# Performance work log

Measured on AMD Instinct MI355X. Metric: run time of the kernel, lower is better.

The kernel has to match this reference:

```python
import jax, jax.numpy as jnp
import numpy as np

N_NODES = 100000
N_EDGES = 1000000
F_IN = 256
HID = 256
HID2 = 128
N_CLS = 2


def setup_inputs() -> dict:
    key = jax.random.key(0)
    ks = jax.random.split(key, 8)
    x = jax.random.normal(ks[0], (N_NODES, F_IN), dtype=jnp.float32)
    edge_index = jax.random.randint(ks[1], (2, N_EDGES), 0, N_NODES, dtype=jnp.int64)
    s = lambda k, shp: jax.random.normal(k, shp, dtype=jnp.float32) / np.sqrt(shp[0])
    return {
        "x": x,
        "edge_index": edge_index,
        "W1l": s(ks[2], (F_IN, HID)),
        "W1r": s(ks[3], (F_IN, HID)),
        "b1": jnp.zeros((HID,), jnp.float32),
        "W2l": s(ks[4], (HID, HID2)),
        "W2r": s(ks[5], (HID, HID2)),
        "b2": jnp.zeros((HID2,), jnp.float32),
        "Wc": s(ks[6], (HID2, N_CLS)),
        "bc": jnp.zeros((N_CLS,), jnp.float32),
    }


def _sage_conv(x, src, dst, deg_inv, Wl, Wr, b):
    # mean-aggregate neighbor (source) features at each destination node
    msg = x[src]                                              # [E, F]
    agg = jax.ops.segment_sum(msg, dst, num_segments=N_NODES)  # [N, F]
    mean = agg * deg_inv[:, None]                             # zero for isolated nodes
    return mean @ Wl + b + x @ Wr


def reference(x, edge_index, W1l, W1r, b1, W2l, W2r, b2, Wc, bc):
    src, dst = edge_index[0], edge_index[1]
    cnt = jax.ops.segment_sum(jnp.ones((N_EDGES,), x.dtype), dst, num_segments=N_NODES)
    deg_inv = jnp.where(cnt > 0, 1.0 / jnp.maximum(cnt, 1.0), 0.0)
    h = jax.nn.relu(_sage_conv(x, src, dst, deg_inv, W1l, W1r, b1))   # dropout is identity in eval
    h = jax.nn.relu(_sage_conv(h, src, dst, deg_inv, W2l, W2r, b2))
    logits = h @ Wc + bc
    return jax.nn.log_softmax(logits, axis=1)
```

## Files before the change

kernel.cpp:

```cpp
#include <hip/hip_runtime.h>
#include <hip/hip_bf16.h>

#define NN 100000
#define NE 1000000
#define MPAD 100096
#define MT64  1564
#define MTP64 1568
#define NG1   (MTP64 * 8)
#define NFB   (NE / 64)
#define NDB   ((NE + 255) / 256)
#define NCB   (MPAD / 8)

typedef __attribute__((ext_vector_type(8))) short bf16x8;
typedef __attribute__((ext_vector_type(4))) float f32x4;
typedef __attribute__((ext_vector_type(2))) float f32x2;
typedef __attribute__((ext_vector_type(8))) unsigned short us8;

static __device__ __forceinline__ float bf2f(unsigned short u){
  unsigned int x = ((unsigned int)u) << 16;
  return __uint_as_float(x);
}
static __device__ __forceinline__ unsigned short f2bf(float f){
  unsigned int x = __float_as_uint(f);
  unsigned int r = (x + 0x7fffu + ((x >> 16) & 1u)) >> 16;
  return (unsigned short)r;
}
static __device__ __forceinline__ void addv(float* acc, us8 v){
  #pragma unroll
  for (int k = 0; k < 8; k++) acc[k] += bf2f(v[k]);
}
static __device__ __forceinline__ unsigned char f2fp8(float f){
  unsigned int u = __float_as_uint(f);
  unsigned int s = (u >> 24) & 0x80u;
  float av = fabsf(f);
  if (av >= 448.f) return (unsigned char)(s | 0x7Eu);
  if (av < 0.015625f){
    int m = (int)(av * 512.0f + 0.5f);
    return (unsigned char)(s | (unsigned)m);
  }
  unsigned int au = u & 0x7FFFFFFFu;
  unsigned int r = au + 0x7FFFFu + ((au >> 20) & 1u);
  return (unsigned char)(s | ((r >> 20) - 960u));
}
#if !__has_builtin(__builtin_amdgcn_cvt_pk_f32_fp8)
static __device__ __forceinline__ float fp8tof(unsigned char b){
  unsigned int s = ((unsigned int)(b & 0x80u)) << 24;
  unsigned int e = (b >> 3) & 0xFu, m = b & 7u;
  float v = (e == 0) ? ((float)m * 0.001953125f)
                     : __uint_as_float(((e + 120u) << 23) | (m << 20));
  return __uint_as_float(__float_as_uint(v) | s);
}
#endif
static __device__ __forceinline__ void addq(float* acc, uint2 v){
#if __has_builtin(__builtin_amdgcn_cvt_pk_f32_fp8)
  f32x2 p0 = __builtin_amdgcn_cvt_pk_f32_fp8((int)v.x, false);
  f32x2 p1 = __builtin_amdgcn_cvt_pk_f32_fp8((int)v.x, true);
  f32x2 p2 = __builtin_amdgcn_cvt_pk_f32_fp8((int)v.y, false);
  f32x2 p3 = __builtin_amdgcn_cvt_pk_f32_fp8((int)v.y, true);
  acc[0] += p0[0]; acc[1] += p0[1]; acc[2] += p1[0]; acc[3] += p1[1];
  acc[4] += p2[0]; acc[5] += p2[1]; acc[6] += p3[0]; acc[7] += p3[1];
#else
  unsigned int a = v.x, b = v.y;
  acc[0] += fp8tof(a & 0xFF);         acc[1] += fp8tof((a >> 8) & 0xFF);
  acc[2] += fp8tof((a >> 16) & 0xFF); acc[3] += fp8tof(a >> 24);
  acc[4] += fp8tof(b & 0xFF);         acc[5] += fp8tof((b >> 8) & 0xFF);
  acc[6] += fp8tof((b >> 16) & 0xFF); acc[7] += fp8tof(b >> 24);
#endif
}
static __device__ __forceinline__ void gld16(const void* g, void* l){
  __builtin_amdgcn_global_load_lds((const __attribute__((address_space(1))) void*)g,
                                   (__attribute__((address_space(3))) void*)l, 16, 0, 0);
}


__global__ __launch_bounds__(256)
void k_dc(const int* __restrict__ dst, int* __restrict__ cnt,
          const float* __restrict__ x, unsigned short* __restrict__ xb,
          const float* __restrict__ W1l, const float* __restrict__ W1r,
          const float* __restrict__ W2l, const float* __restrict__ W2r,
          unsigned short* __restrict__ Bt1, unsigned short* __restrict__ Bt2)
{
  const int bid = blockIdx.x, t = threadIdx.x;
  int role, idx;
  if (bid < 2 * NDB){
    role = bid & 1;
    idx = bid >> 1;
  } else if (bid < NDB + NCB){
    role = 0; idx = bid - NDB;
  } else {
    role = 2; idx = bid - NDB - NCB;
  }

  if (role == 1){
    int e = idx * 256 + t;
    if (e < NE) atomicAdd(&cnt[dst[e]], 1);
  } else if (role == 0){
    size_t i = ((size_t)idx * 256 + t) * 8;
    if (i >= (size_t)MPAD * 256) return;
    int row = (int)(i >> 8);
    us8 o;
    if (row < NN){
      const float4* p = (const float4*)(x + i);
      float4 a = p[0], b = p[1];
      o[0]=f2bf(a.x); o[1]=f2bf(a.y); o[2]=f2bf(a.z); o[3]=f2bf(a.w);
      o[4]=f2bf(b.x); o[5]=f2bf(b.y); o[6]=f2bf(b.z); o[7]=f2bf(b.w);
    } else {
      #pragma unroll
      for (int j = 0; j < 8; j++) o[j] = 0;
    }
    *(us8*)(xb + i) = o;
  } else {
    int i = idx * 256 + t;
    if (i < 512 * 256){
      int n = i >> 8, k = i & 255;
      float v = (n < 256) ? W1l[k * 256 + n] : W1r[k * 256 + (n - 256)];
      Bt1[n * 256 + k] = f2bf(v);
    }
    if (i < 256 * 256){
      int n = i >> 8, k = i & 255;
      float v = (n < 128) ? W2l[k * 128 + n] : W2r[k * 128 + (n - 128)];
      Bt2[n * 256 + k] = f2bf(v);
    }
  }
}


__global__ void k_chunk_sum(const int* __restrict__ cnt, int* __restrict__ partials, int N){
  __shared__ int sw[16];
  int b = blockIdx.x, t = threadIdx.x;
  int i = b * 1024 + t;
  int v = (i < N) ? cnt[i] : 0;
  #pragma unroll
  for (int off = 32; off; off >>= 1) v += __shfl_xor(v, off);
  int lane = t & 63, w = t >> 6;
  if (lane == 0) sw[w] = v;
  __syncthreads();
  if (t < 16){
    int s = sw[t];
    #pragma unroll
    for (int off = 8; off; off >>= 1) s += __shfl_xor(s, off);
    if (t == 0) partials[b] = s;
  }
}

__global__ void k_chunk_scan(const int* __restrict__ cnt, const int* __restrict__ partials,
                             int nchunk,
                             int* __restrict__ offs, int* __restrict__ cursor,
                             float* __restrict__ deginv, int N){
  __shared__ int sd[1024];
  __shared__ int sp[128];
  int b = blockIdx.x, t = threadIdx.x;
  if (t < 128) sp[t] = (t < b && t < nchunk) ? partials[t] : 0;
  int i = b * 1024 + t;
  int v = (i < N) ? cnt[i] : 0;
  sd[t] = v;
  __syncthreads();
  #pragma unroll
  for (int off = 64; off; off >>= 1){
    if (t < off) sp[t] += sp[t + off];
    __syncthreads();
  }
  for (int off = 1; off < 1024; off <<= 1){
    int x = (t >= off) ? sd[t - off] : 0;
    __syncthreads();
    sd[t] += x;
    __syncthreads();
  }
  if (i < N){
    int excl = sp[0] + sd[t] - v;
    offs[i] = excl;
    cursor[i] = excl;
    deginv[i] = (v > 0) ? (1.0f / (float)v) : 0.0f;
  }
}


__global__ __launch_bounds__(64)
void k_fg(const unsigned short* __restrict__ A,
          const unsigned short* __restrict__ Bt,
          unsigned short* __restrict__ R1,
          unsigned char* __restrict__ Q8,
          const int* __restrict__ src, const int* __restrict__ dst,
          int* __restrict__ cursor, int* __restrict__ csr)
{
  __shared__ __align__(16) unsigned short lA[64 * 64];
  __shared__ __align__(16) unsigned short lB[64 * 64];
  const int bid = blockIdx.x;
  const int lane = threadIdx.x & 63;

  bool isg; int idx;
  if (bid < 2 * NG1){
    isg = (bid & 15) < 8;
    idx = ((bid >> 4) << 3) + (bid & 7);
  } else {
    isg = false; idx = bid - NG1;
  }

  if (!isg){
    int e = idx * 64 + lane;
    if (e < NE){
      int p = atomicAdd(&cursor[dst[e]], 1);
      csr[p] = src[e];
    }
    return;
  }

  const int xcd = idx & 7, j = idx >> 3;
  const int mt  = xcd * (MTP64 / 8) + (j >> 3);
  if (mt >= MT64) return;
  const int nt  = j & 7;
  const int m0  = mt * 64;
  const int n0  = nt * 64;

  f32x4 acc[4][4] = {};
  const int srow = lane >> 3;
  const int sc   = (lane & 7) ^ ((lane >> 3) & 7);

  for (int kt = 0; kt < 4; ++kt){
    asm volatile("s_waitcnt lgkmcnt(0)" ::: "memory");
    #pragma unroll
    for (int s = 0; s < 8; ++s){
      int row = s * 8 + srow;
      gld16(A  + (size_t)(m0 + row) * 256 + kt * 64 + sc * 8, &lA[s * 512]);
      gld16(Bt + (size_t)(n0 + row) * 256 + kt * 64 + sc * 8, &lB[s * 512]);
    }
    asm volatile("s_waitcnt vmcnt(0)" ::: "memory");
    __builtin_amdgcn_sched_barrier(0);
    #pragma unroll
    for (int ks = 0; ks < 2; ++ks){
      bf16x8 av[4], bv[4];
      const int kc = ks * 4 + (lane >> 4);
      #pragma unroll
      for (int m = 0; m < 4; m++){
        int r = m * 16 + (lane & 15);
        av[m] = *(const bf16x8*)&lA[r * 64 + ((kc ^ (r & 7)) << 3)];
      }
      #pragma unroll
      for (int n = 0; n < 4; n++){
        int c = n * 16 + (lane & 15);
        bv[n] = *(const bf16x8*)&lB[c * 64 + ((kc ^ (c & 7)) << 3)];
      }
      #pragma unroll
      for (int m = 0; m < 4; m++)
        #pragma unroll
        for (int n = 0; n < 4; n++)
          acc[m][n] = __builtin_amdgcn_mfma_f32_16x16x32_bf16(av[m], bv[n], acc[m][n], 0, 0, 0);
    }
  }

  const int crow0 = m0 + (lane >> 4) * 4;
  const int ccol0 = n0 + (lane & 15);
  if (n0 < 256){
    #pragma unroll
    for (int m = 0; m < 4; m++){
      #pragma unroll
      for (int r = 0; r < 4; r++){
        size_t rowoff = (size_t)(crow0 + m * 16 + r) * 256;
        #pragma unroll
        for (int n = 0; n < 4; n++)
          Q8[rowoff + ccol0 + n * 16] = f2fp8(acc[m][n][r]);
      }
    }
  } else {
    const int cbase = ccol0 - 256;
    #pragma unroll
    for (int m = 0; m < 4; m++){
      #pragma unroll
      for (int r = 0; r < 4; r++){
        size_t rowoff = (size_t)(crow0 + m * 16 + r) * 256;
        #pragma unroll
        for (int n = 0; n < 4; n++)
          R1[rowoff + cbase + n * 16] = f2bf(acc[m][n][r]);
      }
    }
  }
}


template<int NTL2>
__global__ __launch_bounds__(64)
void k_gemm(const unsigned short* __restrict__ A,
            const unsigned short* __restrict__ Bt,
            unsigned short* __restrict__ C)
{
  const int bid = blockIdx.x;
  const int xcd = bid & 7, j = bid >> 3;
  const int mt  = xcd * (MTP64 / 8) + (j >> NTL2);
  if (mt >= MT64) return;
  const int nt  = j & ((1 << NTL2) - 1);
  const int m0  = mt * 64;
  const int n0  = nt * 64;
  const int Nout = 64 << NTL2;

  __shared__ __align__(16) unsigned short lA[64 * 64];
  __shared__ __align__(16) unsigned short lB[64 * 64];
  const int lane = threadIdx.x & 63;

  f32x4 acc[4][4] = {};
  const int srow = lane >> 3;
  const int sc   = (lane & 7) ^ ((lane >> 3) & 7);

  for (int kt = 0; kt < 4; ++kt){
    asm volatile("s_waitcnt lgkmcnt(0)" ::: "memory");
    #pragma unroll
    for (int s = 0; s < 8; ++s){
      int row = s * 8 + srow;
      gld16(A  + (size_t)(m0 + row) * 256 + kt * 64 + sc * 8, &lA[s * 512]);
      gld16(Bt + (size_t)(n0 + row) * 256 + kt * 64 + sc * 8, &lB[s * 512]);
    }
    asm volatile("s_waitcnt vmcnt(0)" ::: "memory");
    __builtin_amdgcn_sched_barrier(0);
    #pragma unroll
    for (int ks = 0; ks < 2; ++ks){
      bf16x8 av[4], bv[4];
      const int kc = ks * 4 + (lane >> 4);
      #pragma unroll
      for (int m = 0; m < 4; m++){
        int r = m * 16 + (lane & 15);
        av[m] = *(const bf16x8*)&lA[r * 64 + ((kc ^ (r & 7)) << 3)];
      }
      #pragma unroll
      for (int n = 0; n < 4; n++){
        int c = n * 16 + (lane & 15);
        bv[n] = *(const bf16x8*)&lB[c * 64 + ((kc ^ (c & 7)) << 3)];
      }
      #pragma unroll
      for (int m = 0; m < 4; m++)
        #pragma unroll
        for (int n = 0; n < 4; n++)
          acc[m][n] = __builtin_amdgcn_mfma_f32_16x16x32_bf16(av[m], bv[n], acc[m][n], 0, 0, 0);
    }
  }

  const int crow0 = m0 + (lane >> 4) * 4;
  const int ccol0 = n0 + (lane & 15);
  #pragma unroll
  for (int m = 0; m < 4; m++){
    #pragma unroll
    for (int r = 0; r < 4; r++){
      size_t rowoff = (size_t)(crow0 + m * 16 + r) * Nout;
      #pragma unroll
      for (int n = 0; n < 4; n++)
        C[rowoff + ccol0 + n * 16] = f2bf(acc[m][n][r]);
    }
  }
}


__global__ void k_agg1(const unsigned char* __restrict__ Q8,
                       const unsigned short* __restrict__ R1,
                       const float* __restrict__ b1,
                       const int* __restrict__ offs, const int* __restrict__ cnt,
                       const float* __restrict__ deginv,
                       const int* __restrict__ csr,
                       unsigned short* __restrict__ h, int N)
{
  int wv = threadIdx.x >> 6, lane = threadIdx.x & 63;
  int n = blockIdx.x * 4 + wv;
  if (n >= N) return;
  int beg = offs[n], d = cnt[n];
  const int g = lane >> 5;
  const int cl = lane & 31;
  const unsigned char* Qb = Q8 + cl * 8;

  float acc[8];
  #pragma unroll
  for (int k = 0; k < 8; k++) acc[k] = 0.f;

  for (int w0 = 0; w0 < d; w0 += 64){
    int wlen = min(d - w0, 64);
    int idx = 0;
    if (lane < wlen) idx = csr[beg + w0 + lane];
    int nIter = (wlen + 15) >> 4;
    for (int t = 0; t < nIter; t++){
      int e0 = t * 16 + g;
      int s0 = __shfl(idx, e0);
      int s1 = __shfl(idx, e0 + 2);
      int s2 = __shfl(idx, e0 + 4);
      int s3 = __shfl(idx, e0 + 6);
      int s4 = __shfl(idx, e0 + 8);
      int s5 = __shfl(idx, e0 + 10);
      int s6 = __shfl(idx, e0 + 12);
      int s7 = __shfl(idx, e0 + 14);
      uint2 v0 = *(const uint2*)(Qb + (size_t)s0 * 256);
      uint2 v1 = *(const uint2*)(Qb + (size_t)s1 * 256);
      uint2 v2 = *(const uint2*)(Qb + (size_t)s2 * 256);
      uint2 v3 = *(const uint2*)(Qb + (size_t)s3 * 256);
      uint2 v4 = *(const uint2*)(Qb + (size_t)s4 * 256);
      uint2 v5 = *(const uint2*)(Qb + (size_t)s5 * 256);
      uint2 v6 = *(const uint2*)(Qb + (size_t)s6 * 256);
      uint2 v7 = *(const uint2*)(Qb + (size_t)s7 * 256);
      if (e0 < wlen)      addq(acc, v0);
      if (e0 + 2 < wlen)  addq(acc, v1);
      if (e0 + 4 < wlen)  addq(acc, v2);
      if (e0 + 6 < wlen)  addq(acc, v3);
      if (e0 + 8 < wlen)  addq(acc, v4);
      if (e0 + 10 < wlen) addq(acc, v5);
      if (e0 + 12 < wlen) addq(acc, v6);
      if (e0 + 14 < wlen) addq(acc, v7);
    }
  }
  #pragma unroll
  for (int k = 0; k < 8; k++) acc[k] += __shfl_xor(acc[k], 32);

  if (lane < 32){
    float di = deginv[n];
    us8 rv = *(const us8*)(R1 + (size_t)n * 256 + cl * 8);
    float4 b0 = *(const float4*)(b1 + cl * 8);
    float4 b4 = *(const float4*)(b1 + cl * 8 + 4);
    float bb[8] = {b0.x, b0.y, b0.z, b0.w, b4.x, b4.y, b4.z, b4.w};
    us8 o;
    #pragma unroll
    for (int k = 0; k < 8; k++)
      o[k] = f2bf(fmaxf(acc[k] * di + bf2f(rv[k]) + bb[k], 0.f));
    *(us8*)(h + (size_t)n * 256 + cl * 8) = o;
  }
}


__global__ void k_agg2cls(const unsigned short* __restrict__ C2,
                          const float* __restrict__ b2,
                          const float* __restrict__ Wc,
                          const float* __restrict__ bc,
                          const int* __restrict__ offs, const int* __restrict__ cnt,
                          const float* __restrict__ deginv,
                          const int* __restrict__ csr,
                          float* __restrict__ out, int N)
{
  int wv = threadIdx.x >> 6, lane = threadIdx.x & 63;
  int n = blockIdx.x * 4 + wv;
  if (n >= N) return;
  int beg = offs[n], d = cnt[n];
  const int g = lane >> 4;
  const int cl = lane & 15;

  float acc[8];
  #pragma unroll
  for (int k = 0; k < 8; k++) acc[k] = 0.f;

  for (int w0 = 0; w0 < d; w0 += 64){
    int wlen = min(d - w0, 64);
    int idx = 0;
    if (lane < wlen) idx = csr[beg + w0 + lane];
    int nIter = (wlen + 31) >> 5;
    for (int t = 0; t < nIter; t++){
      int e0 = t * 32 + g;
      int s0 = __shfl(idx, e0);
      int s1 = __shfl(idx, e0 + 4);
      int s2 = __shfl(idx, e0 + 8);
      int s3 = __shfl(idx, e0 + 12);
      int s4 = __shfl(idx, e0 + 16);
      int s5 = __shfl(idx, e0 + 20);
      int s6 = __shfl(idx, e0 + 24);
      int s7 = __shfl(idx, e0 + 28);
      us8 v0 = *(const us8*)(C2 + (size_t)s0 * 256 + cl * 8);
      us8 v1 = *(const us8*)(C2 + (size_t)s1 * 256 + cl * 8);
      us8 v2 = *(const us8*)(C2 + (size_t)s2 * 256 + cl * 8);
      us8 v3 = *(const us8*)(C2 + (size_t)s3 * 256 + cl * 8);
      us8 v4 = *(const us8*)(C2 + (size_t)s4 * 256 + cl * 8);
      us8 v5 = *(const us8*)(C2 + (size_t)s5 * 256 + cl * 8);
      us8 v6 = *(const us8*)(C2 + (size_t)s6 * 256 + cl * 8);
      us8 v7 = *(const us8*)(C2 + (size_t)s7 * 256 + cl * 8);
      if (e0 < wlen)      addv(acc, v0);
      if (e0 + 4 < wlen)  addv(acc, v1);
      if (e0 + 8 < wlen)  addv(acc, v2);
      if (e0 + 12 < wlen) addv(acc, v3);
      if (e0 + 16 < wlen) addv(acc, v4);
      if (e0 + 20 < wlen) addv(acc, v5);
      if (e0 + 24 < wlen) addv(acc, v6);
      if (e0 + 28 < wlen) addv(acc, v7);
    }
  }
  #pragma unroll
  for (int k = 0; k < 8; k++){
    acc[k] += __shfl_xor(acc[k], 16);
    acc[k] += __shfl_xor(acc[k], 32);
  }

  float di = deginv[n];
  us8 rv = *(const us8*)(C2 + (size_t)n * 256 + 128 + cl * 8);
  float4 b0 = *(const float4*)(b2 + cl * 8);
  float4 b4 = *(const float4*)(b2 + cl * 8 + 4);
  float bb[8] = {b0.x, b0.y, b0.z, b0.w, b4.x, b4.y, b4.z, b4.w};
  float p0 = 0.f, p1 = 0.f;
  #pragma unroll
  for (int k = 0; k < 8; k += 2){
    float h0 = fmaxf(acc[k]     * di + bf2f(rv[k])     + bb[k],     0.f);
    float h1 = fmaxf(acc[k + 1] * di + bf2f(rv[k + 1]) + bb[k + 1], 0.f);
    float4 w = *(const float4*)(Wc + (cl * 8 + k) * 2);
    p0 += h0 * w.x + h1 * w.z;
    p1 += h0 * w.y + h1 * w.w;
  }
  #pragma unroll
  for (int off = 8; off; off >>= 1){
    p0 += __shfl_xor(p0, off);
    p1 += __shfl_xor(p1, off);
  }
  if (lane == 0){
    float z0 = p0 + bc[0], z1 = p1 + bc[1];
    float m = fmaxf(z0, z1);
    float lse = m + logf(expf(z0 - m) + expf(z1 - m));
    out[(size_t)n * 2 + 0] = z0 - lse;
    out[(size_t)n * 2 + 1] = z1 - lse;
  }
}


extern "C" void kernel_launch(void* const* d_in, const int* in_sizes, int n_in,
                              void* d_out, int out_size, void* d_ws, size_t ws_size,
                              hipStream_t stream)
{
  const float* x   = (const float*)d_in[0];
  const int*   ei  = (const int*)d_in[1];
  const float* W1l = (const float*)d_in[2];
  const float* W1r = (const float*)d_in[3];
  const float* b1  = (const float*)d_in[4];
  const float* W2l = (const float*)d_in[5];
  const float* W2r = (const float*)d_in[6];
  const float* b2  = (const float*)d_in[7];
  const float* Wc  = (const float*)d_in[8];
  const float* bc  = (const float*)d_in[9];
  float* out = (float*)d_out;

  const int N = NN, E = NE;
  const int* src = ei;
  const int* dst = ei + E;

  char* ws = (char*)d_ws;
  size_t off = 0;
  auto alloc = [&](size_t bytes) -> void* {
    void* p = ws + off;
    off += (bytes + 255) & ~(size_t)255;
    return p;
  };
  int*   cnt      = (int*)alloc((size_t)N * 4);
  int*   offs     = (int*)alloc((size_t)N * 4);
  int*   cursor   = (int*)alloc((size_t)N * 4);
  float* deginv   = (float*)alloc((size_t)N * 4);
  int*   partials = (int*)alloc(1024);
  int*   csr      = (int*)alloc((size_t)E * 4);
  unsigned short* Bt1 = (unsigned short*)alloc((size_t)512 * 256 * 2);
  unsigned short* Bt2 = (unsigned short*)alloc((size_t)256 * 256 * 2);
  unsigned short* xb  = (unsigned short*)alloc((size_t)MPAD * 256 * 2);
  unsigned char*  Q8  = (unsigned char*)alloc((size_t)MPAD * 256);
  unsigned short* R1  = (unsigned short*)alloc((size_t)MPAD * 256 * 2);

  unsigned short* h  = xb;
  unsigned short* C2 = R1;

  (void)in_sizes; (void)n_in; (void)out_size; (void)ws_size;

  hipMemsetAsync(cnt, 0, (size_t)N * 4, stream);

  k_dc<<<NDB + NCB + 512, 256, 0, stream>>>(dst, cnt, x, xb, W1l, W1r, W2l, W2r, Bt1, Bt2);

  int nchunk = (N + 1023) / 1024;
  k_chunk_sum<<<nchunk, 1024, 0, stream>>>(cnt, partials, N);
  k_chunk_scan<<<nchunk, 1024, 0, stream>>>(cnt, partials, nchunk, offs, cursor, deginv, N);

  k_fg<<<NG1 + NFB, 64, 0, stream>>>(xb, Bt1, R1, Q8, src, dst, cursor, csr);

  k_agg1<<<N / 4, 256, 0, stream>>>(Q8, R1, b1, offs, cnt, deginv, csr, h, N);

  k_gemm<2><<<MTP64 * 4, 64, 0, stream>>>(h, Bt2, C2);
  k_agg2cls<<<N / 4, 256, 0, stream>>>(C2, b2, Wc, bc, offs, cnt, deginv, csr, out, N);
}
```

Before: 303.0 us.

## Partition CSR fill by destination range per XCD-affine block

The CSR scatter blocks inside the fused GEMM kernel now each scan a 512-edge chunk and handle only edges whose destination falls in one of eight node ranges. The range is chosen from the block index modulo 8, so it lines up with the XCD. The goal is to keep the atomic cursor updates and csr writes for a given node range local to one XCD's L2, cutting cross-die atomic traffic. In exchange, every edge's dst is read eight times, and more blocks are launched.

```diff
diff --git a/kernel.cpp b/kernel.cpp
--- a/kernel.cpp
+++ b/kernel.cpp
@@ -7,9 +7,12 @@
 #define MT64  1564
 #define MTP64 1568
 #define NG1   (MTP64 * 8)
-#define NFB   (NE / 64)
 #define NDB   ((NE + 255) / 256)
 #define NCB   (MPAD / 8)
+#define CSZ   512
+#define NCHK  ((NE + CSZ - 1) / CSZ)
+#define CINT  ((2 * NG1) / 16)
+#define NRES  (NN / 8)
 
 typedef __attribute__((ext_vector_type(8))) short bf16x8;
 typedef __attribute__((ext_vector_type(4))) float f32x4;
@@ -188,19 +191,29 @@
   const int bid = blockIdx.x;
   const int lane = threadIdx.x & 63;
 
-  bool isg; int idx;
+  bool isg; int idx = 0, r = 0, c = 0;
   if (bid < 2 * NG1){
-    isg = (bid & 15) < 8;
-    idx = ((bid >> 4) << 3) + (bid & 7);
+    if ((bid & 15) < 8){ isg = true;  idx = ((bid >> 4) << 3) + (bid & 7); }
+    else               { isg = false; r = bid & 7; c = bid >> 4; }
   } else {
-    isg = false; idx = bid - NG1;
+    int t2 = bid - 2 * NG1;
+    isg = false; r = t2 & 7; c = CINT + (t2 >> 3);
   }
 
   if (!isg){
-    int e = idx * 64 + lane;
-    if (e < NE){
-      int p = atomicAdd(&cursor[dst[e]], 1);
-      csr[p] = src[e];
+    if (c < NCHK){
+      int base = c * CSZ;
+      #pragma unroll
+      for (int w = 0; w < CSZ; w += 64){
+        int e = base + w + lane;
+        if (e < NE){
+          int dn = dst[e];
+          if ((unsigned)(dn - r * NRES) < (unsigned)NRES){
+            int p = atomicAdd(&cursor[dn], 1);
+            csr[p] = src[e];
+          }
+        }
+      }
     }
     return;
   }
@@ -232,13 +245,13 @@
       const int kc = ks * 4 + (lane >> 4);
       #pragma unroll
       for (int m = 0; m < 4; m++){
-        int r = m * 16 + (lane & 15);
-        av[m] = *(const bf16x8*)&lA[r * 64 + ((kc ^ (r & 7)) << 3)];
+        int rr = m * 16 + (lane & 15);
+        av[m] = *(const bf16x8*)&lA[rr * 64 + ((kc ^ (rr & 7)) << 3)];
       }
       #pragma unroll
       for (int n = 0; n < 4; n++){
-        int c = n * 16 + (lane & 15);
-        bv[n] = *(const bf16x8*)&lB[c * 64 + ((kc ^ (c & 7)) << 3)];
+        int cc = n * 16 + (lane & 15);
+        bv[n] = *(const bf16x8*)&lB[cc * 64 + ((kc ^ (cc & 7)) << 3)];
       }
       #pragma unroll
       for (int m = 0; m < 4; m++)
@@ -254,11 +267,11 @@
     #pragma unroll
     for (int m = 0; m < 4; m++){
       #pragma unroll
-      for (int r = 0; r < 4; r++){
-        size_t rowoff = (size_t)(crow0 + m * 16 + r) * 256;
+      for (int rr = 0; rr < 4; rr++){
+        size_t rowoff = (size_t)(crow0 + m * 16 + rr) * 256;
         #pragma unroll
         for (int n = 0; n < 4; n++)
-          Q8[rowoff + ccol0 + n * 16] = f2fp8(acc[m][n][r]);
+          Q8[rowoff + ccol0 + n * 16] = f2fp8(acc[m][n][rr]);
       }
     }
   } else {
@@ -266,11 +279,11 @@
     #pragma unroll
     for (int m = 0; m < 4; m++){
       #pragma unroll
-      for (int r = 0; r < 4; r++){
-        size_t rowoff = (size_t)(crow0 + m * 16 + r) * 256;
+      for (int rr = 0; rr < 4; rr++){
+        size_t rowoff = (size_t)(crow0 + m * 16 + rr) * 256;
         #pragma unroll
         for (int n = 0; n < 4; n++)
-          R1[rowoff + cbase + n * 16] = f2bf(acc[m][n][r]);
+          R1[rowoff + cbase + n * 16] = f2bf(acc[m][n][rr]);
       }
     }
   }
@@ -316,13 +329,13 @@
       const int kc = ks * 4 + (lane >> 4);
       #pragma unroll
       for (int m = 0; m < 4; m++){
-        int r = m * 16 + (lane & 15);
-        av[m] = *(const bf16x8*)&lA[r * 64 + ((kc ^ (r & 7)) << 3)];
+        int rr = m * 16 + (lane & 15);
+        av[m] = *(const bf16x8*)&lA[rr * 64 + ((kc ^ (rr & 7)) << 3)];
       }
       #pragma unroll
       for (int n = 0; n < 4; n++){
-        int c = n * 16 + (lane & 15);
-        bv[n] = *(const bf16x8*)&lB[c * 64 + ((kc ^ (c & 7)) << 3)];
+        int cc = n * 16 + (lane & 15);
+        bv[n] = *(const bf16x8*)&lB[cc * 64 + ((kc ^ (cc & 7)) << 3)];
       }
       #pragma unroll
       for (int m = 0; m < 4; m++)
@@ -337,11 +350,11 @@
   #pragma unroll
   for (int m = 0; m < 4; m++){
     #pragma unroll
-    for (int r = 0; r < 4; r++){
-      size_t rowoff = (size_t)(crow0 + m * 16 + r) * Nout;
+    for (int rr = 0; rr < 4; rr++){
+      size_t rowoff = (size_t)(crow0 + m * 16 + rr) * Nout;
       #pragma unroll
       for (int n = 0; n < 4; n++)
-        C[rowoff + ccol0 + n * 16] = f2bf(acc[m][n][r]);
+        C[rowoff + ccol0 + n * 16] = f2bf(acc[m][n][rr]);
     }
   }
 }
@@ -558,7 +571,10 @@
   k_chunk_sum<<<nchunk, 1024, 0, stream>>>(cnt, partials, N);
   k_chunk_scan<<<nchunk, 1024, 0, stream>>>(cnt, partials, nchunk, offs, cursor, deginv, N);
 
-  k_fg<<<NG1 + NFB, 64, 0, stream>>>(xb, Bt1, R1, Q8, src, dst, cursor, csr);
+  {
+    int ntail = 8 * (NCHK - CINT);
+    k_fg<<<2 * NG1 + ntail, 64, 0, stream>>>(xb, Bt1, R1, Q8, src, dst, cursor, csr);
+  }
 
   k_agg1<<<N / 4, 256, 0, stream>>>(Q8, R1, b1, offs, cnt, deginv, csr, h, N);
 
```

Result: no change. 306.6 us (+1.2%).

## Double-buffer LDS tiles in GEMM kernels to overlap loads with MFMA

Applied to the files above, without the earlier changes.

Moves the shared GEMM tile loop into a helper that double-buffers A and B tiles in LDS. The next K-slice is prefetched with direct-to-LDS loads while MFMAs run on the current slice, so load latency is meant to hide behind compute instead of serialising per K step. LDS use per block doubles to 32KB, which may lower occupancy for these single-wave blocks. The partial vmcnt wait relies on the exact number of outstanding loads.

```diff
diff --git a/kernel.cpp b/kernel.cpp
--- a/kernel.cpp
+++ b/kernel.cpp
@@ -175,6 +175,62 @@
 }
 
 
+static __device__ __forceinline__
+void gemm_tile_db(const unsigned short* __restrict__ A,
+                  const unsigned short* __restrict__ Bt,
+                  unsigned short* lA, unsigned short* lB,
+                  int lane, int m0, int n0,
+                  f32x4 (*acc)[4])
+{
+  const int srow = lane >> 3;
+  const int sc   = (lane & 7) ^ ((lane >> 3) & 7);
+  #pragma unroll
+  for (int s = 0; s < 8; ++s){
+    int row = s * 8 + srow;
+    gld16(A  + (size_t)(m0 + row) * 256 + sc * 8, &lA[s * 512]);
+    gld16(Bt + (size_t)(n0 + row) * 256 + sc * 8, &lB[s * 512]);
+  }
+  #pragma unroll
+  for (int kt = 0; kt < 4; ++kt){
+    const int cur = (kt & 1) * 4096;
+    if (kt < 3){
+      const int nxt = ((kt + 1) & 1) * 4096;
+      asm volatile("s_waitcnt lgkmcnt(0)" ::: "memory");
+      #pragma unroll
+      for (int s = 0; s < 8; ++s){
+        int row = s * 8 + srow;
+        gld16(A  + (size_t)(m0 + row) * 256 + (kt + 1) * 64 + sc * 8, &lA[nxt + s * 512]);
+        gld16(Bt + (size_t)(n0 + row) * 256 + (kt + 1) * 64 + sc * 8, &lB[nxt + s * 512]);
+      }
+      asm volatile("s_waitcnt vmcnt(16)" ::: "memory");
+    } else {
+      asm volatile("s_waitcnt vmcnt(0)" ::: "memory");
+    }
+    __builtin_amdgcn_sched_barrier(0);
+    #pragma unroll
+    for (int ks = 0; ks < 2; ++ks){
+      bf16x8 av[4], bv[4];
+      const int kc = ks * 4 + (lane >> 4);
+      #pragma unroll
+      for (int m = 0; m < 4; m++){
+        int r = m * 16 + (lane & 15);
+        av[m] = *(const bf16x8*)&lA[cur + r * 64 + ((kc ^ (r & 7)) << 3)];
+      }
+      #pragma unroll
+      for (int n = 0; n < 4; n++){
+        int c = n * 16 + (lane & 15);
+        bv[n] = *(const bf16x8*)&lB[cur + c * 64 + ((kc ^ (c & 7)) << 3)];
+      }
+      #pragma unroll
+      for (int m = 0; m < 4; m++)
+        #pragma unroll
+        for (int n = 0; n < 4; n++)
+          acc[m][n] = __builtin_amdgcn_mfma_f32_16x16x32_bf16(av[m], bv[n], acc[m][n], 0, 0, 0);
+    }
+  }
+}
+
+
 __global__ __launch_bounds__(64)
 void k_fg(const unsigned short* __restrict__ A,
           const unsigned short* __restrict__ Bt,
@@ -183,8 +239,8 @@
           const int* __restrict__ src, const int* __restrict__ dst,
           int* __restrict__ cursor, int* __restrict__ csr)
 {
-  __shared__ __align__(16) unsigned short lA[64 * 64];
-  __shared__ __align__(16) unsigned short lB[64 * 64];
+  __shared__ __align__(16) unsigned short lA[2 * 64 * 64];
+  __shared__ __align__(16) unsigned short lB[2 * 64 * 64];
   const int bid = blockIdx.x;
   const int lane = threadIdx.x & 63;
 
@@ -213,40 +269,7 @@
   const int n0  = nt * 64;
 
   f32x4 acc[4][4] = {};
-  const int srow = lane >> 3;
-  const int sc   = (lane & 7) ^ ((lane >> 3) & 7);
-
-  for (int kt = 0; kt < 4; ++kt){
-    asm volatile("s_waitcnt lgkmcnt(0)" ::: "memory");
-    #pragma unroll
-    for (int s = 0; s < 8; ++s){
-      int row = s * 8 + srow;
-      gld16(A  + (size_t)(m0 + row) * 256 + kt * 64 + sc * 8, &lA[s * 512]);
-      gld16(Bt + (size_t)(n0 + row) * 256 + kt * 64 + sc * 8, &lB[s * 512]);
-    }
-    asm volatile("s_waitcnt vmcnt(0)" ::: "memory");
-    __builtin_amdgcn_sched_barrier(0);
-    #pragma unroll
-    for (int ks = 0; ks < 2; ++ks){
-      bf16x8 av[4], bv[4];
-      const int kc = ks * 4 + (lane >> 4);
-      #pragma unroll
-      for (int m = 0; m < 4; m++){
-        int r = m * 16 + (lane & 15);
-        av[m] = *(const bf16x8*)&lA[r * 64 + ((kc ^ (r & 7)) << 3)];
-      }
-      #pragma unroll
-      for (int n = 0; n < 4; n++){
-        int c = n * 16 + (lane & 15);
-        bv[n] = *(const bf16x8*)&lB[c * 64 + ((kc ^ (c & 7)) << 3)];
-      }
-      #pragma unroll
-      for (int m = 0; m < 4; m++)
-        #pragma unroll
-        for (int n = 0; n < 4; n++)
-          acc[m][n] = __builtin_amdgcn_mfma_f32_16x16x32_bf16(av[m], bv[n], acc[m][n], 0, 0, 0);
-    }
-  }
+  gemm_tile_db(A, Bt, lA, lB, lane, m0, n0, acc);
 
   const int crow0 = m0 + (lane >> 4) * 4;
   const int ccol0 = n0 + (lane & 15);
@@ -292,45 +315,12 @@
   const int n0  = nt * 64;
   const int Nout = 64 << NTL2;
 
-  __shared__ __align__(16) unsigned short lA[64 * 64];
-  __shared__ __align__(16) unsigned short lB[64 * 64];
+  __shared__ __align__(16) unsigned short lA[2 * 64 * 64];
+  __shared__ __align__(16) unsigned short lB[2 * 64 * 64];
   const int lane = threadIdx.x & 63;
 
   f32x4 acc[4][4] = {};
-  const int srow = lane >> 3;
-  const int sc   = (lane & 7) ^ ((lane >> 3) & 7);
-
-  for (int kt = 0; kt < 4; ++kt){
-    asm volatile("s_waitcnt lgkmcnt(0)" ::: "memory");
-    #pragma unroll
-    for (int s = 0; s < 8; ++s){
-      int row = s * 8 + srow;
-      gld16(A  + (size_t)(m0 + row) * 256 + kt * 64 + sc * 8, &lA[s * 512]);
-      gld16(Bt + (size_t)(n0 + row) * 256 + kt * 64 + sc * 8, &lB[s * 512]);
-    }
-    asm volatile("s_waitcnt vmcnt(0)" ::: "memory");
-    __builtin_amdgcn_sched_barrier(0);
-    #pragma unroll
-    for (int ks = 0; ks < 2; ++ks){
-      bf16x8 av[4], bv[4];
-      const int kc = ks * 4 + (lane >> 4);
-      #pragma unroll
-      for (int m = 0; m < 4; m++){
-        int r = m * 16 + (lane & 15);
-        av[m] = *(const bf16x8*)&lA[r * 64 + ((kc ^ (r & 7)) << 3)];
-      }
-      #pragma unroll
-      for (int n = 0; n < 4; n++){
-        int c = n * 16 + (lane & 15);
-        bv[n] = *(const bf16x8*)&lB[c * 64 + ((kc ^ (c & 7)) << 3)];
-      }
-      #pragma unroll
-      for (int m = 0; m < 4; m++)
-        #pragma unroll
-        for (int n = 0; n < 4; n++)
-          acc[m][n] = __builtin_amdgcn_mfma_f32_16x16x32_bf16(av[m], bv[n], acc[m][n], 0, 0, 0);
-    }
-  }
+  gemm_tile_db(A, Bt, lA, lB, lane, m0, n0, acc);
 
   const int crow0 = m0 + (lane >> 4) * 4;
   const int ccol0 = n0 + (lane & 15);
```

Measured after the change: 358.0 us. 1.18x slower.
